# Optimization experiments

Hardware: AMD Instinct MI355X
Metric: run time of the kernel (lower is better)

The kernel has to match this reference:

```python
import jax, jax.numpy as jnp
import numpy as np

N = 50000      # nodes
K = 17         # regular degree (edges per node, pre-sorted by row)
D_IN = 128
D_OUT = 64
E = N * K


def setup_inputs() -> dict:
    key = jax.random.key(0)
    k1, k2, k3, k4, k5 = jax.random.split(key, 5)
    x = jax.random.normal(k1, (N, D_IN), dtype=jnp.float32)
    # edges sorted by row (required by dimmedian_idx); regular degree K
    row = jnp.repeat(jnp.arange(N, dtype=jnp.int32), K)
    col = jax.random.randint(k2, (E,), 0, N, dtype=jnp.int32)
    edge_index = jnp.stack([row, col], axis=0)
    edge_weight = jax.random.uniform(k3, (E,), dtype=jnp.float32)
    # glorot-style linear weight, zero-init-like small bias
    weight = jax.random.normal(k4, (D_IN, D_OUT), dtype=jnp.float32) * np.float32(1.0 / np.sqrt(D_IN))
    bias = jax.random.normal(k5, (D_OUT,), dtype=jnp.float32) * np.float32(0.01)
    return {"x": x, "edge_index": edge_index, "edge_weight": edge_weight,
            "weight": weight, "bias": bias}


def _weighted_dim_median(xp, col, w):
    """Per-node, per-dimension weighted median over neighbors (dimmedian_idx + gather).
    xp: [N, D] projected features; col: [E] neighbor ids; w: [E] edge weights.
    Exploits the regular degree K: edges for node i occupy rows i*K:(i+1)*K.
    """
    D = xp.shape[1]
    vals = xp[col].reshape(N, K, D)            # neighbor features per node
    wN = jnp.broadcast_to(w.reshape(N, K)[:, :, None], (N, K, D))
    order = jnp.argsort(vals, axis=1)          # sort neighbors per dim by value
    sorted_vals = jnp.take_along_axis(vals, order, axis=1)
    sorted_w = jnp.take_along_axis(wN, order, axis=1)
    cum = jnp.cumsum(sorted_w, axis=1)
    total = cum[:, -1:, :]
    # first sorted position where cumulative weight reaches half the total
    med_pos = jnp.argmax(cum >= 0.5 * total, axis=1)      # [N, D]
    med = jnp.take_along_axis(sorted_vals, med_pos[:, None, :], axis=1)[:, 0, :]
    return med


def reference(x, edge_index, edge_weight, weight, bias):
    xp = x @ weight                            # lin projection (no bias)
    row, col = edge_index[0], edge_index[1]
    med = _weighted_dim_median(xp, col, edge_weight)      # soft_median_reduce
    # row normalization: scatter_add of edge weights per destination row
    row_sum = jax.ops.segment_sum(edge_weight, row, num_segments=N)
    return row_sum[:, None] * med + bias
```

## Files before the change

### kernel.cpp

```cpp
#include <hip/hip_runtime.h>

#define N_NODES 50000
#define K_DEG   17
#define DIN     128
#define DOUT    64

typedef _Float16 f16;
typedef __attribute__((ext_vector_type(8))) short  short8;
typedef __attribute__((ext_vector_type(4))) float  floatx4;

struct CEPair { unsigned char a, b; };

constexpr int net_count(int n) {
  int t = 0; while ((1 << t) < n) ++t;
  int cnt = 0;
  for (int p = 1 << (t - 1); p > 0; p >>= 1) {
    int q = 1 << (t - 1), r = 0, d = p;
    for (;;) {
      for (int i = 0; i < n - d; ++i)
        if ((i & p) == r) ++cnt;
      if (q == p) break;
      d = q - p; q >>= 1; r = p;
    }
  }
  return cnt;
}

template <int NP> struct NetArr { CEPair v[NP]; };

template <int NP>
constexpr NetArr<NP> net_pairs(int n) {
  NetArr<NP> out{};
  int t = 0; while ((1 << t) < n) ++t;
  int cnt = 0;
  for (int p = 1 << (t - 1); p > 0; p >>= 1) {
    int q = 1 << (t - 1), r = 0, d = p;
    for (;;) {
      for (int i = 0; i < n - d; ++i)
        if ((i & p) == r) {
          out.v[cnt].a = (unsigned char)i;
          out.v[cnt].b = (unsigned char)(i + d);
          ++cnt;
        }
      if (q == p) break;
      d = q - p; q >>= 1; r = p;
    }
  }
  return out;
}

constexpr int NP17 = net_count(K_DEG);

__device__ __forceinline__ unsigned int f2bf(float f) {
  union { float f; unsigned int u; } c; c.f = f;
  return (c.u + 0x7FFFu + ((c.u >> 16) & 1u)) >> 16;
}
__device__ __forceinline__ float bf2f(unsigned int b) {
  union { float f; unsigned int u; } c; c.u = b << 16;
  return c.f;
}

__global__ void convw_kernel(const float* __restrict__ W,
                             unsigned short* __restrict__ T) {
  const int flat = blockIdx.x * 256 + threadIdx.x;
  const int j    = flat & 7;
  const int lane = (flat >> 3) & 63;
  const int pair = flat >> 9;
  const int ks   = pair >> 2, nt = pair & 3;
  const int k    = ks * 32 + (lane >> 4) * 8 + j;
  const int n    = nt * 16 + (lane & 15);
  const float f  = W[k * DOUT + n];
  const unsigned int hb = f2bf(f);
  const float        lo = f - bf2f(hb);
  const unsigned int lb = f2bf(lo);
  T[flat]        = (unsigned short)hb;
  T[flat + 8192] = (unsigned short)lb;
}

__global__ __launch_bounds__(256) void gemm_kernel(
    const float* __restrict__ x, const unsigned short* __restrict__ T,
    f16* __restrict__ xp) {
  const int gwave = blockIdx.x * 4 + (threadIdx.x >> 6);
  if (gwave >= (N_NODES / 16)) return;
  const int lane = threadIdx.x & 63;
  const int r0 = gwave * 16;
  const int m  = lane & 15;
  const int q  = lane >> 4;

  const float4* x4 = (const float4*)x;
  float4 xr[8];
  #pragma unroll
  for (int ks = 0; ks < 4; ++ks) {
    const int base = (r0 + m) * (DIN / 4) + ks * 8 + q * 2;
    xr[ks * 2 + 0] = x4[base + 0];
    xr[ks * 2 + 1] = x4[base + 1];
  }

  floatx4 acc[4];
  #pragma unroll
  for (int nt = 0; nt < 4; ++nt) acc[nt] = (floatx4){0.f, 0.f, 0.f, 0.f};

  const short8* Th = (const short8*)T;
  const short8* Tl = (const short8*)(T + 8192);

  #pragma unroll
  for (int ks = 0; ks < 4; ++ks) {
    short8 Bh[4], Bl[4];
    #pragma unroll
    for (int nt = 0; nt < 4; ++nt) {
      const int fi = (ks * 4 + nt) * 64 + lane;
      Bh[nt] = Th[fi];
      Bl[nt] = Tl[fi];
    }
    float f[8] = {xr[ks*2].x, xr[ks*2].y, xr[ks*2].z, xr[ks*2].w,
                  xr[ks*2+1].x, xr[ks*2+1].y, xr[ks*2+1].z, xr[ks*2+1].w};
    union { unsigned int i[4]; short8 s; } Ah, Al;
    #pragma unroll
    for (int r = 0; r < 4; ++r) {
      const unsigned int h0 = f2bf(f[2*r]),   h1 = f2bf(f[2*r+1]);
      const unsigned int l0 = f2bf(f[2*r]   - bf2f(h0));
      const unsigned int l1 = f2bf(f[2*r+1] - bf2f(h1));
      Ah.i[r] = h0 | (h1 << 16);
      Al.i[r] = l0 | (l1 << 16);
    }
    #pragma unroll
    for (int nt = 0; nt < 4; ++nt) {
      acc[nt] = __builtin_amdgcn_mfma_f32_16x16x32_bf16(Al.s, Bh[nt], acc[nt], 0, 0, 0);
      acc[nt] = __builtin_amdgcn_mfma_f32_16x16x32_bf16(Ah.s, Bl[nt], acc[nt], 0, 0, 0);
      acc[nt] = __builtin_amdgcn_mfma_f32_16x16x32_bf16(Ah.s, Bh[nt], acc[nt], 0, 0, 0);
    }
  }

  #pragma unroll
  for (int nt = 0; nt < 4; ++nt) {
    const int col = nt * 16 + m;
    #pragma unroll
    for (int r = 0; r < 4; ++r)
      xp[(r0 + q * 4 + r) * DOUT + col] = (f16)acc[nt][r];
  }
}

__global__ __launch_bounds__(256, 2) void median_kernel(
    const f16* __restrict__ xp, const int* __restrict__ col,
    const float* __restrict__ ew, const float* __restrict__ bias,
    float* __restrict__ out) {
  __shared__ float wlds[4 * K_DEG * 64];

  const int wave = threadIdx.x >> 6;
  const int lane = threadIdx.x & 63;
  const int node = __builtin_amdgcn_readfirstlane(blockIdx.x * 4 + wave);

  const int*   cp = col + node * K_DEG;
  const float* wp = ew  + node * K_DEG;

  int c[K_DEG];
  #pragma unroll
  for (int j = 0; j < K_DEG; ++j) c[j] = cp[j];

  float v[K_DEG];
  #pragma unroll
  for (int j = 0; j < K_DEG; ++j)
    v[j] = (float)xp[c[j] * DOUT + lane];

  float* wl = wlds + wave * (K_DEG * 64) + lane;
  #pragma unroll
  for (int j = 0; j < K_DEG; ++j) wl[j * 64] = wp[j];

  const float bl = bias[lane];

  #pragma unroll
  for (int j = 0; j < K_DEG; ++j) {
    union { float f; unsigned int u; } c2; c2.f = v[j];
    c2.u |= (unsigned)j;
    v[j] = c2.f;
  }

  constexpr NetArr<NP17> NET = net_pairs<NP17>(K_DEG);
  #pragma unroll
  for (int s = 0; s < NP17; ++s) {
    const int a = NET.v[s].a, b = NET.v[s].b;
    const float va = v[a], vb = v[b];
    v[a] = fminf(va, vb);
    v[b] = fmaxf(va, vb);
  }

  float sw[K_DEG];
  #pragma unroll
  for (int j = 0; j < K_DEG; ++j) {
    union { float f; unsigned int u; } c2; c2.f = v[j];
    sw[j] = wl[(c2.u & 31u) * 64];
  }

  float cum[K_DEG];
  float run = 0.f;
  #pragma unroll
  for (int j = 0; j < K_DEG; ++j) { run += sw[j]; cum[j] = run; }
  const float half = 0.5f * run;

  float med = v[K_DEG - 1];
  #pragma unroll
  for (int j = K_DEG - 2; j >= 0; --j)
    med = (cum[j] >= half) ? v[j] : med;

  out[node * DOUT + lane] = run * med + bl;
}

extern "C" void kernel_launch(void* const* d_in, const int* in_sizes, int n_in,
                              void* d_out, int out_size, void* d_ws, size_t ws_size,
                              hipStream_t stream) {
  const float* x    = (const float*)d_in[0];
  const int*   ei   = (const int*)d_in[1];
  const float* ew   = (const float*)d_in[2];
  const float* W    = (const float*)d_in[3];
  const float* bias = (const float*)d_in[4];
  float*       out  = (float*)d_out;

  f16*            xp = (f16*)d_ws;
  unsigned short* T  = (unsigned short*)((char*)d_ws + (size_t)N_NODES * DOUT * 2);
  const int*      colp = ei + (size_t)N_NODES * K_DEG;

  convw_kernel<<<8192 / 256, 256, 0, stream>>>(W, T);
  gemm_kernel<<<(N_NODES / 16 + 3) / 4, 256, 0, stream>>>(x, T, xp);
  median_kernel<<<N_NODES / 4, 256, 0, stream>>>(xp, colp, ew, bias, out);
}
```

Measured before the change: 122.4 us.

## Process two nodes per wave in median kernel with compact LDS weight table

Each wave now handles two nodes instead of one, interleaving two independent 17-element sorting networks to raise instruction-level parallelism and halve the grid size. Edge weights are stored once per wave (34 floats) in LDS rather than replicated per lane, cutting LDS footprint and store traffic. The weight lookup uses the tag bits shifted by 2 as a byte offset directly. Register pressure roughly doubles, which could reduce occupancy under the launch bound of 2 blocks per CU.

```diff
diff --git a/kernel.cpp b/kernel.cpp
--- a/kernel.cpp
+++ b/kernel.cpp
@@ -144,65 +144,88 @@
     const f16* __restrict__ xp, const int* __restrict__ col,
     const float* __restrict__ ew, const float* __restrict__ bias,
     float* __restrict__ out) {
-  __shared__ float wlds[4 * K_DEG * 64];
+  __shared__ float wlds[4 * 64];
 
   const int wave = threadIdx.x >> 6;
   const int lane = threadIdx.x & 63;
-  const int node = __builtin_amdgcn_readfirstlane(blockIdx.x * 4 + wave);
-
-  const int*   cp = col + node * K_DEG;
-  const float* wp = ew  + node * K_DEG;
-
-  int c[K_DEG];
-  #pragma unroll
-  for (int j = 0; j < K_DEG; ++j) c[j] = cp[j];
-
-  float v[K_DEG];
-  #pragma unroll
-  for (int j = 0; j < K_DEG; ++j)
-    v[j] = (float)xp[c[j] * DOUT + lane];
-
-  float* wl = wlds + wave * (K_DEG * 64) + lane;
-  #pragma unroll
-  for (int j = 0; j < K_DEG; ++j) wl[j * 64] = wp[j];
+  const int node0 = __builtin_amdgcn_readfirstlane((blockIdx.x * 4 + wave) * 2);
+
+  const int*   cp = col + node0 * K_DEG;
+  const float* wp = ew  + node0 * K_DEG;
+
+  int c0[K_DEG], c1[K_DEG];
+  #pragma unroll
+  for (int j = 0; j < K_DEG; ++j) { c0[j] = cp[j]; c1[j] = cp[K_DEG + j]; }
+
+  float v0[K_DEG], v1[K_DEG];
+  #pragma unroll
+  for (int j = 0; j < K_DEG; ++j) v0[j] = (float)xp[c0[j] * DOUT + lane];
+  #pragma unroll
+  for (int j = 0; j < K_DEG; ++j) v1[j] = (float)xp[c1[j] * DOUT + lane];
+
+  {
+    float* wb = wlds + wave * 64;
+    if (lane < 2 * K_DEG) {
+      const float wv = wp[lane];
+      const int   a  = (lane < K_DEG) ? lane : (32 + lane - K_DEG);
+      wb[a] = wv;
+    }
+  }
 
   const float bl = bias[lane];
 
   #pragma unroll
   for (int j = 0; j < K_DEG; ++j) {
-    union { float f; unsigned int u; } c2; c2.f = v[j];
-    c2.u |= (unsigned)j;
-    v[j] = c2.f;
+    union { float f; unsigned int u; } a, b;
+    a.f = v0[j]; a.u |= (unsigned)(j * 4); v0[j] = a.f;
+    b.f = v1[j]; b.u |= (unsigned)(j * 4); v1[j] = b.f;
   }
 
   constexpr NetArr<NP17> NET = net_pairs<NP17>(K_DEG);
   #pragma unroll
   for (int s = 0; s < NP17; ++s) {
     const int a = NET.v[s].a, b = NET.v[s].b;
-    const float va = v[a], vb = v[b];
-    v[a] = fminf(va, vb);
-    v[b] = fmaxf(va, vb);
-  }
-
-  float sw[K_DEG];
-  #pragma unroll
-  for (int j = 0; j < K_DEG; ++j) {
-    union { float f; unsigned int u; } c2; c2.f = v[j];
-    sw[j] = wl[(c2.u & 31u) * 64];
-  }
-
-  float cum[K_DEG];
-  float run = 0.f;
-  #pragma unroll
-  for (int j = 0; j < K_DEG; ++j) { run += sw[j]; cum[j] = run; }
-  const float half = 0.5f * run;
-
-  float med = v[K_DEG - 1];
-  #pragma unroll
-  for (int j = K_DEG - 2; j >= 0; --j)
-    med = (cum[j] >= half) ? v[j] : med;
-
-  out[node * DOUT + lane] = run * med + bl;
+    const float x0 = v0[a], y0 = v0[b];
+    v0[a] = fminf(x0, y0);  v0[b] = fmaxf(x0, y0);
+    const float x1 = v1[a], y1 = v1[b];
+    v1[a] = fminf(x1, y1);  v1[b] = fmaxf(x1, y1);
+  }
+
+  const unsigned base0 = (unsigned)(wave * 256);
+  const unsigned base1 = base0 + 128;
+  const char* wbytes = (const char*)wlds;
+
+  {
+    float run = 0.f, cum[K_DEG];
+    #pragma unroll
+    for (int j = 0; j < K_DEG; ++j) {
+      union { float f; unsigned int u; } a; a.f = v0[j];
+      const float swj = *(const float*)(wbytes + ((a.u & 0x7Cu) | base0));
+      run += swj; cum[j] = run;
+    }
+    const float half = 0.5f * run;
+    float med = v0[K_DEG - 1];
+    #pragma unroll
+    for (int j = K_DEG - 2; j >= 0; --j)
+      med = (cum[j] >= half) ? v0[j] : med;
+    out[node0 * DOUT + lane] = run * med + bl;
+  }
+
+  {
+    float run = 0.f, cum[K_DEG];
+    #pragma unroll
+    for (int j = 0; j < K_DEG; ++j) {
+      union { float f; unsigned int u; } a; a.f = v1[j];
+      const float swj = *(const float*)(wbytes + ((a.u & 0x7Cu) | base1));
+      run += swj; cum[j] = run;
+    }
+    const float half = 0.5f * run;
+    float med = v1[K_DEG - 1];
+    #pragma unroll
+    for (int j = K_DEG - 2; j >= 0; --j)
+      med = (cum[j] >= half) ? v1[j] : med;
+    out[(node0 + 1) * DOUT + lane] = run * med + bl;
+  }
 }
 
 extern "C" void kernel_launch(void* const* d_in, const int* in_sizes, int n_in,
@@ -221,5 +244,5 @@
 
   convw_kernel<<<8192 / 256, 256, 0, stream>>>(W, T);
   gemm_kernel<<<(N_NODES / 16 + 3) / 4, 256, 0, stream>>>(x, T, xp);
-  median_kernel<<<N_NODES / 4, 256, 0, stream>>>(xp, colp, ew, bias, out);
-}
+  median_kernel<<<N_NODES / 8, 256, 0, stream>>>(xp, colp, ew, bias, out);
+}
```

Result: no change. 120.3 us (-1.8%).
